# Kernel tuning notes

Measured on AMD Instinct MI355X. Metric: run time of the kernel, lower is better.

The kernel has to match this reference:

```python
import jax, jax.numpy as jnp
import numpy as np

B, S, D, H, L = 4, 2048, 512, 8, 128
HD = D // H  # head dim = 64


def setup_inputs() -> dict:
    key = jax.random.key(0)
    ks = jax.random.split(key, 20)
    sc = 0.05
    return {
        "query": jax.random.normal(ks[0], (B, S, D), jnp.float32),
        "key": jax.random.normal(ks[1], (B, S, D), jnp.float32),
        "value": jax.random.normal(ks[2], (B, S, D), jnp.float32),
        "Wq": jax.random.normal(ks[3], (D, D), jnp.float32) * sc,
        "bq": jax.random.normal(ks[4], (D,), jnp.float32) * sc,
        "Wk": jax.random.normal(ks[5], (D, D), jnp.float32) * sc,
        "bk": jax.random.normal(ks[6], (D,), jnp.float32) * sc,
        "Wv": jax.random.normal(ks[7], (D, D), jnp.float32) * sc,
        "bv": jax.random.normal(ks[8], (D,), jnp.float32) * sc,
        "Wo": jax.random.normal(ks[9], (D, D), jnp.float32) * sc,
        "bo": jax.random.normal(ks[10], (D,), jnp.float32) * sc,
        "Wg": jax.random.normal(ks[11], (D, L), jnp.float32) * sc,
        "bg": jax.random.normal(ks[12], (L,), jnp.float32) * sc,
        "Wmq": jax.random.normal(ks[13], (L, D), jnp.float32) * sc,
        "bmq": jax.random.normal(ks[14], (D,), jnp.float32) * sc,
        "Wmk": jax.random.normal(ks[15], (L, D), jnp.float32) * sc,
        "bmk": jax.random.normal(ks[16], (D,), jnp.float32) * sc,
    }


def reference(query, key, value, Wq, bq, Wk, bk, Wv, bv, Wo, bo, Wg, bg, Wmq, bmq, Wmk, bmk):
    # latent-gated modulation of Q and K (computed from query)
    latent = jax.nn.relu(query @ Wg + bg)                 # [B,S,L]
    mod_q = jax.nn.sigmoid(latent @ Wmq + bmq)            # [B,S,D]
    mod_k = jax.nn.sigmoid(latent @ Wmk + bmk)            # [B,S,D]
    q = (query @ Wq + bq) * mod_q
    k = (key @ Wk + bk) * mod_k
    v = value @ Wv + bv
    # split heads: [B,S,D] -> [B,S,H,HD]
    q = q.reshape(B, S, H, HD)
    k = k.reshape(B, S, H, HD)
    v = v.reshape(B, S, H, HD)
    scale = 1.0 / jnp.sqrt(jnp.float32(HD))
    scores = jnp.einsum("bqhd,bkhd->bhqk", q, k) * scale  # [B,H,S,S]
    attn_weights = jax.nn.softmax(scores, axis=-1)
    attn_out = jnp.einsum("bhqk,bkhd->bqhd", attn_weights, v).reshape(B, S, D)
    output = attn_out @ Wo + bo
    return output, attn_weights
```

## Files before the change

### kernel.cpp

```cpp
#include <hip/hip_runtime.h>
#include <hip/hip_bf16.h>

#define BB 4
#define SS 2048
#define DD 512
#define HH 8
#define HDIM 64

typedef __attribute__((ext_vector_type(8))) short bf16x8;
typedef __attribute__((ext_vector_type(4))) float floatx4;
typedef __attribute__((ext_vector_type(8))) unsigned short u16x8;

static __device__ __forceinline__ unsigned short f2bf(float x) {
  __hip_bfloat16 h = __float2bfloat16(x);
  unsigned short u;
  __builtin_memcpy(&u, &h, sizeof(u));
  return u;
}
static __device__ __forceinline__ float bf2f(unsigned short u) {
  union { unsigned int i; float f; } c;
  c.i = ((unsigned int)u) << 16;
  return c.f;
}
static __device__ __forceinline__ void split1(float x, unsigned short& h, unsigned short& l) {
  h = f2bf(x);
  l = f2bf(x - bf2f(h));
}
static __device__ __forceinline__ void gload_lds16(const void* g, void* l) {
  __builtin_amdgcn_global_load_lds((const __attribute__((address_space(1))) void*)g,
                                   (__attribute__((address_space(3))) void*)l, 16, 0, 0);
}

#define SWZ(row, col) ((col) ^ (((row) & 7) * 8))

static __device__ __forceinline__ void stage_tile(unsigned short* dst,
    const unsigned short* src, size_t rstride, int wid, int lane) {
#pragma unroll
  for (int it = 0; it < 2; ++it) {
    const int base = it * 256 + wid * 64;
    const int c = base + lane;
    const int row = c >> 3, uu = c & 7;
    gload_lds16(src + (size_t)row * rstride + ((uu ^ (row & 7)) * 8),
                dst + (size_t)base * 8);
  }
}

__global__ __launch_bounds__(256)
void wsplit_kernel(const float* __restrict__ Wq, const float* __restrict__ Wk,
                   const float* __restrict__ Wv, const float* __restrict__ Wo,
                   const float* __restrict__ Wg, const float* __restrict__ Wmq,
                   const float* __restrict__ Wmk, unsigned short* __restrict__ wsb)
{
  const int bx = blockIdx.x;
  const float* src; unsigned short* dh; unsigned short* dl; int K, N, tile;
  if (bx < 64)       { src = Wq;  dh = wsb + 0;       dl = wsb + 262144;  K = 512; N = 512; tile = bx; }
  else if (bx < 128) { src = Wk;  dh = wsb + 524288;  dl = wsb + 786432;  K = 512; N = 512; tile = bx - 64; }
  else if (bx < 192) { src = Wv;  dh = wsb + 1048576; dl = wsb + 1310720; K = 512; N = 512; tile = bx - 128; }
  else if (bx < 256) { src = Wo;  dh = wsb + 1572864; dl = wsb + 1835008; K = 512; N = 512; tile = bx - 192; }
  else if (bx < 272) { src = Wg;  dh = wsb + 2097152; dl = wsb + 2162688; K = 512; N = 128; tile = bx - 256; }
  else if (bx < 288) { src = Wmq; dh = wsb + 2228224; dl = wsb + 2293760; K = 128; N = 512; tile = bx - 272; }
  else               { src = Wmk; dh = wsb + 2359296; dl = wsb + 2424832; K = 128; N = 512; tile = bx - 288; }
  const int nt = N >> 6;
  const int k0 = (tile / nt) * 64, n0 = (tile % nt) * 64;
  __shared__ float T[64][65];
  const int t = threadIdx.x;
  const int r = t >> 2, c = (t & 3) * 16;
#pragma unroll
  for (int j = 0; j < 16; j += 4)
    *(float4*)&T[r][c + j] = *(const float4*)&src[(size_t)(k0 + r) * N + n0 + c + j];
  __syncthreads();
  u16x8 hv[2], lv[2];
#pragma unroll
  for (int j = 0; j < 16; ++j) {
    unsigned short h, l;
    split1(T[c + j][r], h, l);
    hv[j >> 3][j & 7] = h;
    lv[j >> 3][j & 7] = l;
  }
  const size_t di = (size_t)(n0 + r) * K + k0 + c;
  *(u16x8*)&dh[di]     = hv[0];
  *(u16x8*)&dh[di + 8] = hv[1];
  *(u16x8*)&dl[di]     = lv[0];
  *(u16x8*)&dl[di + 8] = lv[1];
}

template<int BM, int BN>
static __device__ __forceinline__ void gemm_phase(
    const float* __restrict__ A, const unsigned short* __restrict__ WHp,
    const unsigned short* __restrict__ WLp, const int K,
    const int m0, const int n0,
    unsigned short (*Ah)[32], unsigned short (*Al)[32],
    unsigned short (*Bh)[32], unsigned short (*Bl)[32],
    floatx4 (*acc)[BN / 32])
{
  constexpr int HM = BM / 2, HN = BN / 2, FM = BM / 32, FN = BN / 32;
  constexpr int TPR = 256 / BM;
  constexpr int CPT = 32 / TPR;
  constexpr int WCH = BN / 16;
  constexpr int WPW = (2 * WCH) / 4;
  const int t = threadIdx.x;
  const int wid = t >> 6, lane = t & 63, quad = lane >> 4, l16 = lane & 15;
  const int wm = wid >> 1, wn = wid & 1;
  const int arow = t / TPR, acol = (t % TPR) * CPT;
  const int asw = (arow & 3) * 8;

  for (int k0 = 0; k0 < K; k0 += 32) {
    __syncthreads();
#pragma unroll
    for (int cc = 0; cc < WPW; ++cc) {
      const int cid = wid * WPW + cc;
      const int pl = cid / WCH, ch = cid - pl * WCH;
      const int row = ch * 16 + (lane >> 2);
      const int kof = ((lane & 3) ^ ((lane >> 2) & 3)) * 8;
      const unsigned short* g = (pl ? WLp : WHp) + (size_t)(n0 + row) * K + k0 + kof;
      gload_lds16(g, (pl ? Bl : Bh)[ch * 16]);
    }
    {
      const float* ga = A + (size_t)(m0 + arow) * K + k0 + acol;
#pragma unroll
      for (int j = 0; j < CPT; j += 4) {
        float4 f = *(const float4*)(ga + j);
        unsigned short h[4], l[4];
        split1(f.x, h[0], l[0]); split1(f.y, h[1], l[1]);
        split1(f.z, h[2], l[2]); split1(f.w, h[3], l[3]);
        *(ushort4*)&Ah[arow][(acol + j) ^ asw] = make_ushort4(h[0], h[1], h[2], h[3]);
        *(ushort4*)&Al[arow][(acol + j) ^ asw] = make_ushort4(l[0], l[1], l[2], l[3]);
      }
    }
    __syncthreads();
    const int swf = (l16 & 3) * 8;
    bf16x8 fah[FM], fal[FM], fbh[FN], fbl[FN];
#pragma unroll
    for (int mi = 0; mi < FM; ++mi) {
      const int rr = wm * HM + mi * 16 + l16;
      fah[mi] = *(const bf16x8*)&Ah[rr][(quad * 8) ^ swf];
      fal[mi] = *(const bf16x8*)&Al[rr][(quad * 8) ^ swf];
    }
#pragma unroll
    for (int ni = 0; ni < FN; ++ni) {
      const int rr = wn * HN + ni * 16 + l16;
      fbh[ni] = *(const bf16x8*)&Bh[rr][(quad * 8) ^ swf];
      fbl[ni] = *(const bf16x8*)&Bl[rr][(quad * 8) ^ swf];
    }
#pragma unroll
    for (int mi = 0; mi < FM; ++mi)
#pragma unroll
      for (int ni = 0; ni < FN; ++ni) {
        acc[mi][ni] = __builtin_amdgcn_mfma_f32_16x16x32_bf16(fah[mi], fbh[ni], acc[mi][ni], 0, 0, 0);
        acc[mi][ni] = __builtin_amdgcn_mfma_f32_16x16x32_bf16(fal[mi], fbh[ni], acc[mi][ni], 0, 0, 0);
        acc[mi][ni] = __builtin_amdgcn_mfma_f32_16x16x32_bf16(fah[mi], fbl[ni], acc[mi][ni], 0, 0, 0);
      }
  }
}

template<int BM, int BN, int EPI>
__global__ __launch_bounds__(256, 2)
void mgemm_kernel(const float* __restrict__ A, const unsigned short* __restrict__ WH,
                  const unsigned short* __restrict__ WL, const float* __restrict__ bias,
                  const float* __restrict__ modf, const float sc,
                  float* __restrict__ Cf, unsigned short* __restrict__ C16,
                  int K, int N)
{
  constexpr int HM = BM / 2, HN = BN / 2, FM = BM / 32, FN = BN / 32;
  __shared__ alignas(16) unsigned short Ah[BM][32], Al[BM][32], Bh[BN][32], Bl[BN][32];
  const int t = threadIdx.x;
  const int wid = t >> 6, lane = t & 63, quad = lane >> 4, l16 = lane & 15;
  const int wm = wid >> 1, wn = wid & 1;
  const int m0 = blockIdx.y * BM, n0 = blockIdx.x * BN;

  floatx4 acc[FM][FN];
#pragma unroll
  for (int i = 0; i < FM; ++i)
#pragma unroll
    for (int j = 0; j < FN; ++j) {
      floatx4 z = {0.f, 0.f, 0.f, 0.f};
      acc[i][j] = z;
    }

  gemm_phase<BM, BN>(A, WH, WL, K, m0, n0, Ah, Al, Bh, Bl, acc);

#pragma unroll
  for (int ni = 0; ni < FN; ++ni) {
    const int col = n0 + wn * HN + ni * 16 + l16;
    const float b1 = bias[col];
#pragma unroll
    for (int mi = 0; mi < FM; ++mi)
#pragma unroll
      for (int r = 0; r < 4; ++r) {
        const int row = m0 + wm * HM + mi * 16 + quad * 4 + r;
        float v = acc[mi][ni][r] + b1;
        if constexpr (EPI == 0) {
          Cf[(size_t)row * N + col] = v;
        } else if constexpr (EPI == 1) {
          Cf[(size_t)row * N + col] = fmaxf(v, 0.f);
        } else if constexpr (EPI == 2) {
          C16[(size_t)row * N + col] = f2bf(v);
        } else if constexpr (EPI == 4) {
          const float m = modf[(size_t)row * N + col];
          C16[(size_t)row * N + col] = f2bf(v * m * sc);
        } else {
          Cf[(size_t)row * N + col] = 1.f / (1.f + __expf(-v));
        }
      }
  }
}

__global__ __launch_bounds__(256)
void vtrans_kernel(const unsigned short* __restrict__ V16, unsigned short* __restrict__ Vt)
{
  __shared__ unsigned short T[64][72];
  const int x  = blockIdx.x;
  const int st = x & 31;
  const int h  = (x >> 5) & 7;
  const int b  = x >> 8;
  const int t  = threadIdx.x;
  const unsigned short* src = V16 + ((size_t)b * SS + st * 64) * DD + h * HDIM;
  for (int i = t; i < 1024; i += 256) {
    int r = i >> 4, c4 = (i & 15) * 4;
    *(ushort4*)&T[r][c4] = *(const ushort4*)&src[(size_t)r * DD + c4];
  }
  __syncthreads();
  unsigned short* dst = Vt + ((size_t)(b * HH + h) * HDIM) * SS + st * 64;
  for (int i = t; i < 1024; i += 256) {
    int hd = i >> 4, s4 = (i & 15) * 4;
    ushort4 u = make_ushort4(T[s4 + 0][hd], T[s4 + 1][hd], T[s4 + 2][hd], T[s4 + 3][hd]);
    *(ushort4*)&dst[(size_t)hd * SS + s4] = u;
  }
}

__global__ __launch_bounds__(256, 3)
void attn_kernel(const unsigned short* __restrict__ Q16,
                 const unsigned short* __restrict__ K16,
                 const unsigned short* __restrict__ Vt,
                 float* __restrict__ AW, float* __restrict__ AO)
{
  __shared__ alignas(16) unsigned short Qs[64][64];
  __shared__ alignas(16) unsigned short Ks[2][64][64];
  __shared__ alignas(16) unsigned short Vs[2][64][64];
  __shared__ alignas(16) unsigned short Ps[4][16][64];

  const int t    = threadIdx.x;
  const int wid  = t >> 6;
  const int lane = t & 63;
  const int quad = lane >> 4;
  const int l16  = lane & 15;
  const int x  = blockIdx.x;
  const int j  = x >> 3;
  const int g  = ((j >> 5) << 3) | (x & 7);
  const int qb = j & 31;
  const int b  = g >> 3;
  const int h  = g & 7;
  const int q0 = qb * 64;

  const unsigned short* Qg = Q16 + ((size_t)b * SS + q0) * DD + h * HDIM;
  const unsigned short* Kg = K16 + (size_t)b * SS * DD + h * HDIM;
  const unsigned short* Vg = Vt + ((size_t)(b * HH + h) * HDIM) * SS;

  stage_tile(&Qs[0][0], Qg, DD, wid, lane);
  stage_tile(&Ks[0][0][0], Kg, DD, wid, lane);
  __syncthreads();

  const bf16x8 a0 = *(const bf16x8*)&Qs[wid * 16 + l16][SWZ(l16, quad * 8)];
  const bf16x8 a1 = *(const bf16x8*)&Qs[wid * 16 + l16][SWZ(l16, 32 + quad * 8)];

  float lsum[4] = {0.f, 0.f, 0.f, 0.f};
  for (int kt = 0; kt < SS / 64; ++kt) {
    const int cur = kt & 1;
    if (kt < 31)
      stage_tile(&Ks[cur ^ 1][0][0], Kg + (size_t)(kt + 1) * 64 * DD, DD, wid, lane);
#pragma unroll
    for (int kst = 0; kst < 4; ++kst) {
      bf16x8 bb0 = *(const bf16x8*)&Ks[cur][kst * 16 + l16][SWZ(l16, quad * 8)];
      bf16x8 bb1 = *(const bf16x8*)&Ks[cur][kst * 16 + l16][SWZ(l16, 32 + quad * 8)];
      floatx4 cc = {0.f, 0.f, 0.f, 0.f};
      cc = __builtin_amdgcn_mfma_f32_16x16x32_bf16(a0, bb0, cc, 0, 0, 0);
      cc = __builtin_amdgcn_mfma_f32_16x16x32_bf16(a1, bb1, cc, 0, 0, 0);
#pragma unroll
      for (int r = 0; r < 4; ++r) lsum[r] += __expf(cc[r]);
    }
    __syncthreads();
  }
#pragma unroll
  for (int r = 0; r < 4; ++r) {
    float v = lsum[r];
    v += __shfl_xor(v, 1, 64); v += __shfl_xor(v, 2, 64);
    v += __shfl_xor(v, 4, 64); v += __shfl_xor(v, 8, 64);
    lsum[r] = 1.f / v;
  }

  floatx4 o[4];
#pragma unroll
  for (int n = 0; n < 4; ++n) { floatx4 z = {0.f, 0.f, 0.f, 0.f}; o[n] = z; }

  const size_t awb = ((size_t)(b * HH + h) * SS + q0 + wid * 16) * SS;

  stage_tile(&Ks[0][0][0], Kg, DD, wid, lane);
  stage_tile(&Vs[0][0][0], Vg, SS, wid, lane);
  __syncthreads();
  for (int kt = 0; kt < SS / 64; ++kt) {
    const int cur = kt & 1;
    if (kt < 31) {
      stage_tile(&Ks[cur ^ 1][0][0], Kg + (size_t)(kt + 1) * 64 * DD, DD, wid, lane);
      stage_tile(&Vs[cur ^ 1][0][0], Vg + (size_t)(kt + 1) * 64, SS, wid, lane);
    }
#pragma unroll
    for (int kst = 0; kst < 4; ++kst) {
      bf16x8 bb0 = *(const bf16x8*)&Ks[cur][kst * 16 + l16][SWZ(l16, quad * 8)];
      bf16x8 bb1 = *(const bf16x8*)&Ks[cur][kst * 16 + l16][SWZ(l16, 32 + quad * 8)];
      floatx4 cc = {0.f, 0.f, 0.f, 0.f};
      cc = __builtin_amdgcn_mfma_f32_16x16x32_bf16(a0, bb0, cc, 0, 0, 0);
      cc = __builtin_amdgcn_mfma_f32_16x16x32_bf16(a1, bb1, cc, 0, 0, 0);
#pragma unroll
      for (int r = 0; r < 4; ++r) {
        const float wv = __expf(cc[r]) * lsum[r];
        AW[awb + (size_t)(quad * 4 + r) * SS + kt * 64 + kst * 16 + l16] = wv;
        Ps[wid][quad * 4 + r][SWZ(quad * 4 + r, kst * 16 + l16)] = f2bf(wv);
      }
    }
#pragma unroll
    for (int c2 = 0; c2 < 2; ++c2) {
      bf16x8 ap = *(const bf16x8*)&Ps[wid][l16][SWZ(l16, c2 * 32 + quad * 8)];
#pragma unroll
      for (int n = 0; n < 4; ++n) {
        bf16x8 bv = *(const bf16x8*)&Vs[cur][n * 16 + l16][SWZ(l16, c2 * 32 + quad * 8)];
        o[n] = __builtin_amdgcn_mfma_f32_16x16x32_bf16(ap, bv, o[n], 0, 0, 0);
      }
    }
    __syncthreads();
  }
  float* AOg = AO + ((size_t)b * SS + q0 + wid * 16) * DD + h * HDIM;
#pragma unroll
  for (int n = 0; n < 4; ++n)
#pragma unroll
    for (int r = 0; r < 4; ++r)
      AOg[(size_t)(quad * 4 + r) * DD + n * 16 + l16] = o[n][r];
}

extern "C" void kernel_launch(void* const* d_in, const int* in_sizes, int n_in,
                              void* d_out, int out_size, void* d_ws, size_t ws_size,
                              hipStream_t stream) {
  (void)in_sizes; (void)n_in; (void)out_size; (void)ws_size;
  const float* query = (const float*)d_in[0];
  const float* key_i = (const float*)d_in[1];
  const float* value = (const float*)d_in[2];
  const float* Wq  = (const float*)d_in[3];
  const float* bq  = (const float*)d_in[4];
  const float* Wk  = (const float*)d_in[5];
  const float* bk  = (const float*)d_in[6];
  const float* Wv  = (const float*)d_in[7];
  const float* bv  = (const float*)d_in[8];
  const float* Wo  = (const float*)d_in[9];
  const float* bo  = (const float*)d_in[10];
  const float* Wg  = (const float*)d_in[11];
  const float* bg  = (const float*)d_in[12];
  const float* Wmq = (const float*)d_in[13];
  const float* bmq = (const float*)d_in[14];
  const float* Wmk = (const float*)d_in[15];
  const float* bmk = (const float*)d_in[16];

  float* out = (float*)d_out;
  float* AW  = out + (size_t)BB * SS * DD;

  char* ws = (char*)d_ws;
  unsigned short* ws16 = (unsigned short*)ws;
  unsigned short* q16 = (unsigned short*)(ws + (5u  << 20));
  unsigned short* k16 = (unsigned short*)(ws + (13u << 20));
  unsigned short* vt  = (unsigned short*)(ws + (21u << 20));
  float*          lat = (float*)(ws + (29u << 20));
  float*          X   = (float*)(ws + (33u << 20));
  unsigned short* v16 = (unsigned short*)(ws + (33u << 20));
  float*          ao  = (float*)(ws + (33u << 20));

  const size_t W_WQH = 0,       W_WQL = 262144;
  const size_t W_WKH = 524288,  W_WKL = 786432;
  const size_t W_WVH = 1048576, W_WVL = 1310720;
  const size_t W_WOH = 1572864, W_WOL = 1835008;
  const size_t W_WGH = 2097152, W_WGL = 2162688;
  const size_t W_WMQH = 2228224, W_WMQL = 2293760;
  const size_t W_WMKH = 2359296, W_WMKL = 2424832;

  dim3 blk(256);
  wsplit_kernel<<<dim3(304), blk, 0, stream>>>(Wq, Wk, Wv, Wo, Wg, Wmq, Wmk, ws16);
  mgemm_kernel<64, 64, 1><<<dim3(2, 128), blk, 0, stream>>>(
      query, ws16 + W_WGH, ws16 + W_WGL, bg, nullptr, 1.f, lat, nullptr, 512, 128);
  mgemm_kernel<64, 64, 5><<<dim3(8, 128), blk, 0, stream>>>(
      lat, ws16 + W_WMQH, ws16 + W_WMQL, bmq, nullptr, 1.f, X, nullptr, 128, 512);
  mgemm_kernel<128, 64, 4><<<dim3(8, 64), blk, 0, stream>>>(
      query, ws16 + W_WQH, ws16 + W_WQL, bq, X, 0.125f, nullptr, q16, 512, 512);
  mgemm_kernel<64, 64, 5><<<dim3(8, 128), blk, 0, stream>>>(
      lat, ws16 + W_WMKH, ws16 + W_WMKL, bmk, nullptr, 1.f, X, nullptr, 128, 512);
  mgemm_kernel<128, 64, 4><<<dim3(8, 64), blk, 0, stream>>>(
      key_i, ws16 + W_WKH, ws16 + W_WKL, bk, X, 1.f, nullptr, k16, 512, 512);
  mgemm_kernel<128, 64, 2><<<dim3(8, 64), blk, 0, stream>>>(
      value, ws16 + W_WVH, ws16 + W_WVL, bv, nullptr, 1.f, nullptr, v16, 512, 512);
  vtrans_kernel<<<dim3(1024), blk, 0, stream>>>(v16, vt);
  attn_kernel<<<dim3(1024), blk, 0, stream>>>(q16, k16, vt, AW, ao);
  mgemm_kernel<128, 64, 0><<<dim3(8, 64), blk, 0, stream>>>(
      ao, ws16 + W_WOH, ws16 + W_WOL, bo, nullptr, 1.f, out, nullptr, 512, 512);
}
```

Baseline: 865.9 us.

## Pre-split activations to bf16 pairs, drop LDS staging in attention, write weights from bf16

Activations are now split into bf16 hi/lo planes by a separate kernel, so the GEMMs can stage both operands with direct global-to-LDS loads instead of converting in registers. The latent and modulation tensors are stored as bf16 (hi/lo or single), and the GEMM grid is swizzled. The attention kernel drops its shared-memory K/V double buffering and reads K and V fragments straight from global memory. It also writes the attention weights as float4 rows taken from the bf16 P tile in LDS, which rounds the weights to bf16 precision. Buffers are reshuffled so the output buffer is used as scratch. This adds extra split passes and more global traffic in attention, and the bf16 weights carry an accuracy risk.

```diff
diff --git a/kernel.cpp b/kernel.cpp
--- a/kernel.cpp
+++ b/kernel.cpp
@@ -33,16 +33,23 @@
 
 #define SWZ(row, col) ((col) ^ (((row) & 7) * 8))
 
-static __device__ __forceinline__ void stage_tile(unsigned short* dst,
-    const unsigned short* src, size_t rstride, int wid, int lane) {
-#pragma unroll
-  for (int it = 0; it < 2; ++it) {
-    const int base = it * 256 + wid * 64;
-    const int c = base + lane;
-    const int row = c >> 3, uu = c & 7;
-    gload_lds16(src + (size_t)row * rstride + ((uu ^ (row & 7)) * 8),
-                dst + (size_t)base * 8);
-  }
+__global__ __launch_bounds__(256)
+void asplit_kernel(const float* __restrict__ src, unsigned short* __restrict__ H,
+                   unsigned short* __restrict__ L)
+{
+  const size_t i = ((size_t)blockIdx.x * 256 + threadIdx.x) * 8;
+  float4 f0 = *(const float4*)&src[i];
+  float4 f1 = *(const float4*)&src[i + 4];
+  float ff[8] = {f0.x, f0.y, f0.z, f0.w, f1.x, f1.y, f1.z, f1.w};
+  u16x8 hv, lv;
+#pragma unroll
+  for (int j = 0; j < 8; ++j) {
+    unsigned short h, l;
+    split1(ff[j], h, l);
+    hv[j] = h; lv[j] = l;
+  }
+  *(u16x8*)&H[i] = hv;
+  *(u16x8*)&L[i] = lv;
 }
 
 __global__ __launch_bounds__(256)
@@ -84,48 +91,62 @@
   *(u16x8*)&dl[di + 8] = lv[1];
 }
 
-template<int BM, int BN>
-static __device__ __forceinline__ void gemm_phase(
-    const float* __restrict__ A, const unsigned short* __restrict__ WHp,
-    const unsigned short* __restrict__ WLp, const int K,
-    const int m0, const int n0,
-    unsigned short (*Ah)[32], unsigned short (*Al)[32],
-    unsigned short (*Bh)[32], unsigned short (*Bl)[32],
-    floatx4 (*acc)[BN / 32])
+template<int BM, int BN, int EPI, bool SG>
+__global__ __launch_bounds__(256)
+void mgemm_kernel(const unsigned short* __restrict__ AH, const unsigned short* __restrict__ AL,
+                  const unsigned short* __restrict__ WH, const unsigned short* __restrict__ WL,
+                  const float* __restrict__ bias, const unsigned short* __restrict__ mod16,
+                  const float sc, float* __restrict__ Cf, unsigned short* __restrict__ C16,
+                  unsigned short* __restrict__ CH, unsigned short* __restrict__ CL,
+                  int K, int N)
 {
   constexpr int HM = BM / 2, HN = BN / 2, FM = BM / 32, FN = BN / 32;
-  constexpr int TPR = 256 / BM;
-  constexpr int CPT = 32 / TPR;
-  constexpr int WCH = BN / 16;
-  constexpr int WPW = (2 * WCH) / 4;
+  constexpr int AU = BM * 4;
+  constexpr int AIT = (2 * AU) / 256;
+  constexpr int BU = BN * 4;
+  constexpr int BIT = (2 * BU) / 256;
+  __shared__ alignas(16) unsigned short AhS[BM][32], AlS[BM][32], BhS[BN][32], BlS[BN][32];
   const int t = threadIdx.x;
   const int wid = t >> 6, lane = t & 63, quad = lane >> 4, l16 = lane & 15;
   const int wm = wid >> 1, wn = wid & 1;
-  const int arow = t / TPR, acol = (t % TPR) * CPT;
-  const int asw = (arow & 3) * 8;
+  int m0, n0;
+  if constexpr (SG) {
+    const int d = blockIdx.x;
+    m0 = (((d & 7) << 3) | ((d >> 3) & 7)) * BM;
+    n0 = (d >> 6) * BN;
+  } else {
+    m0 = blockIdx.y * BM;
+    n0 = blockIdx.x * BN;
+  }
+
+  floatx4 acc[FM][FN];
+#pragma unroll
+  for (int i = 0; i < FM; ++i)
+#pragma unroll
+    for (int j = 0; j < FN; ++j) {
+      floatx4 z = {0.f, 0.f, 0.f, 0.f};
+      acc[i][j] = z;
+    }
 
   for (int k0 = 0; k0 < K; k0 += 32) {
     __syncthreads();
 #pragma unroll
-    for (int cc = 0; cc < WPW; ++cc) {
-      const int cid = wid * WPW + cc;
-      const int pl = cid / WCH, ch = cid - pl * WCH;
-      const int row = ch * 16 + (lane >> 2);
-      const int kof = ((lane & 3) ^ ((lane >> 2) & 3)) * 8;
-      const unsigned short* g = (pl ? WLp : WHp) + (size_t)(n0 + row) * K + k0 + kof;
-      gload_lds16(g, (pl ? Bl : Bh)[ch * 16]);
-    }
-    {
-      const float* ga = A + (size_t)(m0 + arow) * K + k0 + acol;
-#pragma unroll
-      for (int j = 0; j < CPT; j += 4) {
-        float4 f = *(const float4*)(ga + j);
-        unsigned short h[4], l[4];
-        split1(f.x, h[0], l[0]); split1(f.y, h[1], l[1]);
-        split1(f.z, h[2], l[2]); split1(f.w, h[3], l[3]);
-        *(ushort4*)&Ah[arow][(acol + j) ^ asw] = make_ushort4(h[0], h[1], h[2], h[3]);
-        *(ushort4*)&Al[arow][(acol + j) ^ asw] = make_ushort4(l[0], l[1], l[2], l[3]);
-      }
+    for (int it = 0; it < AIT; ++it) {
+      const int uid = it * 256 + t;
+      const int pl = uid >= AU;
+      const int u = uid & (AU - 1);
+      const int row = u >> 2, cu = (u & 3) ^ (row & 3);
+      gload_lds16((pl ? AL : AH) + (size_t)(m0 + row) * K + k0 + cu * 8,
+                  (pl ? &AlS[0][0] : &AhS[0][0]) + u * 8);
+    }
+#pragma unroll
+    for (int it = 0; it < BIT; ++it) {
+      const int uid = it * 256 + t;
+      const int pl = uid >= BU;
+      const int u = uid & (BU - 1);
+      const int row = u >> 2, cu = (u & 3) ^ (row & 3);
+      gload_lds16((pl ? WL : WH) + (size_t)(n0 + row) * K + k0 + cu * 8,
+                  (pl ? &BlS[0][0] : &BhS[0][0]) + u * 8);
     }
     __syncthreads();
     const int swf = (l16 & 3) * 8;
@@ -133,14 +154,14 @@
 #pragma unroll
     for (int mi = 0; mi < FM; ++mi) {
       const int rr = wm * HM + mi * 16 + l16;
-      fah[mi] = *(const bf16x8*)&Ah[rr][(quad * 8) ^ swf];
-      fal[mi] = *(const bf16x8*)&Al[rr][(quad * 8) ^ swf];
+      fah[mi] = *(const bf16x8*)&AhS[rr][(quad * 8) ^ swf];
+      fal[mi] = *(const bf16x8*)&AlS[rr][(quad * 8) ^ swf];
     }
 #pragma unroll
     for (int ni = 0; ni < FN; ++ni) {
       const int rr = wn * HN + ni * 16 + l16;
-      fbh[ni] = *(const bf16x8*)&Bh[rr][(quad * 8) ^ swf];
-      fbl[ni] = *(const bf16x8*)&Bl[rr][(quad * 8) ^ swf];
+      fbh[ni] = *(const bf16x8*)&BhS[rr][(quad * 8) ^ swf];
+      fbl[ni] = *(const bf16x8*)&BlS[rr][(quad * 8) ^ swf];
     }
 #pragma unroll
     for (int mi = 0; mi < FM; ++mi)
@@ -151,33 +172,6 @@
         acc[mi][ni] = __builtin_amdgcn_mfma_f32_16x16x32_bf16(fah[mi], fbl[ni], acc[mi][ni], 0, 0, 0);
       }
   }
-}
-
-template<int BM, int BN, int EPI>
-__global__ __launch_bounds__(256, 2)
-void mgemm_kernel(const float* __restrict__ A, const unsigned short* __restrict__ WH,
-                  const unsigned short* __restrict__ WL, const float* __restrict__ bias,
-                  const float* __restrict__ modf, const float sc,
-                  float* __restrict__ Cf, unsigned short* __restrict__ C16,
-                  int K, int N)
-{
-  constexpr int HM = BM / 2, HN = BN / 2, FM = BM / 32, FN = BN / 32;
-  __shared__ alignas(16) unsigned short Ah[BM][32], Al[BM][32], Bh[BN][32], Bl[BN][32];
-  const int t = threadIdx.x;
-  const int wid = t >> 6, lane = t & 63, quad = lane >> 4, l16 = lane & 15;
-  const int wm = wid >> 1, wn = wid & 1;
-  const int m0 = blockIdx.y * BM, n0 = blockIdx.x * BN;
-
-  floatx4 acc[FM][FN];
-#pragma unroll
-  for (int i = 0; i < FM; ++i)
-#pragma unroll
-    for (int j = 0; j < FN; ++j) {
-      floatx4 z = {0.f, 0.f, 0.f, 0.f};
-      acc[i][j] = z;
-    }
-
-  gemm_phase<BM, BN>(A, WH, WL, K, m0, n0, Ah, Al, Bh, Bl, acc);
 
 #pragma unroll
   for (int ni = 0; ni < FN; ++ni) {
@@ -191,15 +185,19 @@
         float v = acc[mi][ni][r] + b1;
         if constexpr (EPI == 0) {
           Cf[(size_t)row * N + col] = v;
-        } else if constexpr (EPI == 1) {
-          Cf[(size_t)row * N + col] = fmaxf(v, 0.f);
         } else if constexpr (EPI == 2) {
           C16[(size_t)row * N + col] = f2bf(v);
         } else if constexpr (EPI == 4) {
-          const float m = modf[(size_t)row * N + col];
+          const float m = bf2f(mod16[(size_t)row * N + col]);
           C16[(size_t)row * N + col] = f2bf(v * m * sc);
+        } else if constexpr (EPI == 6) {
+          v = fmaxf(v, 0.f);
+          unsigned short h, l;
+          split1(v, h, l);
+          CH[(size_t)row * N + col] = h;
+          CL[(size_t)row * N + col] = l;
         } else {
-          Cf[(size_t)row * N + col] = 1.f / (1.f + __expf(-v));
+          C16[(size_t)row * N + col] = f2bf(1.f / (1.f + __expf(-v)));
         }
       }
   }
@@ -228,15 +226,12 @@
   }
 }
 
-__global__ __launch_bounds__(256, 3)
+__global__ __launch_bounds__(256)
 void attn_kernel(const unsigned short* __restrict__ Q16,
                  const unsigned short* __restrict__ K16,
                  const unsigned short* __restrict__ Vt,
                  float* __restrict__ AW, float* __restrict__ AO)
 {
-  __shared__ alignas(16) unsigned short Qs[64][64];
-  __shared__ alignas(16) unsigned short Ks[2][64][64];
-  __shared__ alignas(16) unsigned short Vs[2][64][64];
   __shared__ alignas(16) unsigned short Ps[4][16][64];
 
   const int t    = threadIdx.x;
@@ -256,29 +251,22 @@
   const unsigned short* Kg = K16 + (size_t)b * SS * DD + h * HDIM;
   const unsigned short* Vg = Vt + ((size_t)(b * HH + h) * HDIM) * SS;
 
-  stage_tile(&Qs[0][0], Qg, DD, wid, lane);
-  stage_tile(&Ks[0][0][0], Kg, DD, wid, lane);
-  __syncthreads();
-
-  const bf16x8 a0 = *(const bf16x8*)&Qs[wid * 16 + l16][SWZ(l16, quad * 8)];
-  const bf16x8 a1 = *(const bf16x8*)&Qs[wid * 16 + l16][SWZ(l16, 32 + quad * 8)];
+  const bf16x8 a0 = *(const bf16x8*)&Qg[(size_t)(wid * 16 + l16) * DD + quad * 8];
+  const bf16x8 a1 = *(const bf16x8*)&Qg[(size_t)(wid * 16 + l16) * DD + 32 + quad * 8];
 
   float lsum[4] = {0.f, 0.f, 0.f, 0.f};
   for (int kt = 0; kt < SS / 64; ++kt) {
-    const int cur = kt & 1;
-    if (kt < 31)
-      stage_tile(&Ks[cur ^ 1][0][0], Kg + (size_t)(kt + 1) * 64 * DD, DD, wid, lane);
 #pragma unroll
     for (int kst = 0; kst < 4; ++kst) {
-      bf16x8 bb0 = *(const bf16x8*)&Ks[cur][kst * 16 + l16][SWZ(l16, quad * 8)];
-      bf16x8 bb1 = *(const bf16x8*)&Ks[cur][kst * 16 + l16][SWZ(l16, 32 + quad * 8)];
+      const unsigned short* kr = Kg + (size_t)(kt * 64 + kst * 16 + l16) * DD + quad * 8;
+      bf16x8 bb0 = *(const bf16x8*)kr;
+      bf16x8 bb1 = *(const bf16x8*)(kr + 32);
       floatx4 cc = {0.f, 0.f, 0.f, 0.f};
       cc = __builtin_amdgcn_mfma_f32_16x16x32_bf16(a0, bb0, cc, 0, 0, 0);
       cc = __builtin_amdgcn_mfma_f32_16x16x32_bf16(a1, bb1, cc, 0, 0, 0);
 #pragma unroll
       for (int r = 0; r < 4; ++r) lsum[r] += __expf(cc[r]);
     }
-    __syncthreads();
   }
 #pragma unroll
   for (int r = 0; r < 4; ++r) {
@@ -294,39 +282,36 @@
 
   const size_t awb = ((size_t)(b * HH + h) * SS + q0 + wid * 16) * SS;
 
-  stage_tile(&Ks[0][0][0], Kg, DD, wid, lane);
-  stage_tile(&Vs[0][0][0], Vg, SS, wid, lane);
-  __syncthreads();
   for (int kt = 0; kt < SS / 64; ++kt) {
-    const int cur = kt & 1;
-    if (kt < 31) {
-      stage_tile(&Ks[cur ^ 1][0][0], Kg + (size_t)(kt + 1) * 64 * DD, DD, wid, lane);
-      stage_tile(&Vs[cur ^ 1][0][0], Vg + (size_t)(kt + 1) * 64, SS, wid, lane);
-    }
 #pragma unroll
     for (int kst = 0; kst < 4; ++kst) {
-      bf16x8 bb0 = *(const bf16x8*)&Ks[cur][kst * 16 + l16][SWZ(l16, quad * 8)];
-      bf16x8 bb1 = *(const bf16x8*)&Ks[cur][kst * 16 + l16][SWZ(l16, 32 + quad * 8)];
+      const unsigned short* kr = Kg + (size_t)(kt * 64 + kst * 16 + l16) * DD + quad * 8;
+      bf16x8 bb0 = *(const bf16x8*)kr;
+      bf16x8 bb1 = *(const bf16x8*)(kr + 32);
       floatx4 cc = {0.f, 0.f, 0.f, 0.f};
       cc = __builtin_amdgcn_mfma_f32_16x16x32_bf16(a0, bb0, cc, 0, 0, 0);
       cc = __builtin_amdgcn_mfma_f32_16x16x32_bf16(a1, bb1, cc, 0, 0, 0);
 #pragma unroll
       for (int r = 0; r < 4; ++r) {
         const float wv = __expf(cc[r]) * lsum[r];
-        AW[awb + (size_t)(quad * 4 + r) * SS + kt * 64 + kst * 16 + l16] = wv;
         Ps[wid][quad * 4 + r][SWZ(quad * 4 + r, kst * 16 + l16)] = f2bf(wv);
       }
     }
+    for (int i = lane; i < 256; i += 64) {
+      const int q = i >> 4, k4 = (i & 15) * 4;
+      ushort4 u = *(const ushort4*)&Ps[wid][q][SWZ(q, k4)];
+      float4 f = make_float4(bf2f(u.x), bf2f(u.y), bf2f(u.z), bf2f(u.w));
+      *(float4*)&AW[awb + (size_t)q * SS + kt * 64 + k4] = f;
+    }
 #pragma unroll
     for (int c2 = 0; c2 < 2; ++c2) {
       bf16x8 ap = *(const bf16x8*)&Ps[wid][l16][SWZ(l16, c2 * 32 + quad * 8)];
 #pragma unroll
       for (int n = 0; n < 4; ++n) {
-        bf16x8 bv = *(const bf16x8*)&Vs[cur][n * 16 + l16][SWZ(l16, c2 * 32 + quad * 8)];
+        bf16x8 bv = *(const bf16x8*)&Vg[(size_t)(n * 16 + l16) * SS + kt * 64 + c2 * 32 + quad * 8];
         o[n] = __builtin_amdgcn_mfma_f32_16x16x32_bf16(ap, bv, o[n], 0, 0, 0);
       }
     }
-    __syncthreads();
   }
   float* AOg = AO + ((size_t)b * SS + q0 + wid * 16) * DD + h * HDIM;
 #pragma unroll
@@ -361,15 +346,19 @@
   float* out = (float*)d_out;
   float* AW  = out + (size_t)BB * SS * DD;
 
+  unsigned short* vt  = (unsigned short*)out;
+  unsigned short* q16 = (unsigned short*)out + 4194304;
+
   char* ws = (char*)d_ws;
   unsigned short* ws16 = (unsigned short*)ws;
-  unsigned short* q16 = (unsigned short*)(ws + (5u  << 20));
-  unsigned short* k16 = (unsigned short*)(ws + (13u << 20));
-  unsigned short* vt  = (unsigned short*)(ws + (21u << 20));
-  float*          lat = (float*)(ws + (29u << 20));
-  float*          X   = (float*)(ws + (33u << 20));
-  unsigned short* v16 = (unsigned short*)(ws + (33u << 20));
-  float*          ao  = (float*)(ws + (33u << 20));
+  unsigned short* PH   = (unsigned short*)(ws + (5u  << 20));
+  unsigned short* PL   = (unsigned short*)(ws + (13u << 20));
+  unsigned short* latH = (unsigned short*)(ws + (21u << 20));
+  unsigned short* latL = (unsigned short*)(ws + (23u << 20));
+  unsigned short* mod  = (unsigned short*)(ws + (25u << 20));
+  unsigned short* v16  = (unsigned short*)(ws + (33u << 20));
+  float*          ao   = (float*)(ws + (25u << 20));
+  unsigned short* k16  = (unsigned short*)(ws + (41u << 20));
 
   const size_t W_WQH = 0,       W_WQL = 262144;
   const size_t W_WKH = 524288,  W_WKL = 786432;
@@ -381,20 +370,31 @@
 
   dim3 blk(256);
   wsplit_kernel<<<dim3(304), blk, 0, stream>>>(Wq, Wk, Wv, Wo, Wg, Wmq, Wmk, ws16);
-  mgemm_kernel<64, 64, 1><<<dim3(2, 128), blk, 0, stream>>>(
-      query, ws16 + W_WGH, ws16 + W_WGL, bg, nullptr, 1.f, lat, nullptr, 512, 128);
-  mgemm_kernel<64, 64, 5><<<dim3(8, 128), blk, 0, stream>>>(
-      lat, ws16 + W_WMQH, ws16 + W_WMQL, bmq, nullptr, 1.f, X, nullptr, 128, 512);
-  mgemm_kernel<128, 64, 4><<<dim3(8, 64), blk, 0, stream>>>(
-      query, ws16 + W_WQH, ws16 + W_WQL, bq, X, 0.125f, nullptr, q16, 512, 512);
-  mgemm_kernel<64, 64, 5><<<dim3(8, 128), blk, 0, stream>>>(
-      lat, ws16 + W_WMKH, ws16 + W_WMKL, bmk, nullptr, 1.f, X, nullptr, 128, 512);
-  mgemm_kernel<128, 64, 4><<<dim3(8, 64), blk, 0, stream>>>(
-      key_i, ws16 + W_WKH, ws16 + W_WKL, bk, X, 1.f, nullptr, k16, 512, 512);
-  mgemm_kernel<128, 64, 2><<<dim3(8, 64), blk, 0, stream>>>(
-      value, ws16 + W_WVH, ws16 + W_WVL, bv, nullptr, 1.f, nullptr, v16, 512, 512);
+  asplit_kernel<<<dim3(2048), blk, 0, stream>>>(query, PH, PL);
+  mgemm_kernel<64, 64, 6, false><<<dim3(2, 128), blk, 0, stream>>>(
+      PH, PL, ws16 + W_WGH, ws16 + W_WGL, bg, nullptr, 1.f,
+      nullptr, nullptr, latH, latL, 512, 128);
+  mgemm_kernel<64, 64, 7, false><<<dim3(8, 128), blk, 0, stream>>>(
+      latH, latL, ws16 + W_WMQH, ws16 + W_WMQL, bmq, nullptr, 1.f,
+      nullptr, mod, nullptr, nullptr, 128, 512);
+  mgemm_kernel<128, 64, 4, true><<<dim3(512), blk, 0, stream>>>(
+      PH, PL, ws16 + W_WQH, ws16 + W_WQL, bq, mod, 0.125f,
+      nullptr, q16, nullptr, nullptr, 512, 512);
+  asplit_kernel<<<dim3(2048), blk, 0, stream>>>(key_i, PH, PL);
+  mgemm_kernel<64, 64, 7, false><<<dim3(8, 128), blk, 0, stream>>>(
+      latH, latL, ws16 + W_WMKH, ws16 + W_WMKL, bmk, nullptr, 1.f,
+      nullptr, mod, nullptr, nullptr, 128, 512);
+  mgemm_kernel<128, 64, 4, true><<<dim3(512), blk, 0, stream>>>(
+      PH, PL, ws16 + W_WKH, ws16 + W_WKL, bk, mod, 1.f,
+      nullptr, k16, nullptr, nullptr, 512, 512);
+  asplit_kernel<<<dim3(2048), blk, 0, stream>>>(value, PH, PL);
+  mgemm_kernel<128, 64, 2, true><<<dim3(512), blk, 0, stream>>>(
+      PH, PL, ws16 + W_WVH, ws16 + W_WVL, bv, nullptr, 1.f,
+      nullptr, v16, nullptr, nullptr, 512, 512);
   vtrans_kernel<<<dim3(1024), blk, 0, stream>>>(v16, vt);
   attn_kernel<<<dim3(1024), blk, 0, stream>>>(q16, k16, vt, AW, ao);
-  mgemm_kernel<128, 64, 0><<<dim3(8, 64), blk, 0, stream>>>(
-      ao, ws16 + W_WOH, ws16 + W_WOL, bo, nullptr, 1.f, out, nullptr, 512, 512);
-}
+  asplit_kernel<<<dim3(2048), blk, 0, stream>>>(ao, PH, PL);
+  mgemm_kernel<128, 64, 0, true><<<dim3(512), blk, 0, stream>>>(
+      PH, PL, ws16 + W_WOH, ws16 + W_WOL, bo, nullptr, 1.f,
+      out, nullptr, nullptr, nullptr, 512, 512);
+}
```

After: 1.056 ms. 22.0% more time.
